# Kernel tuning notes

Measured on AMD Instinct MI355X. Metric: run time of the kernel, lower is better.

## Reference

```python
import jax, jax.numpy as jnp
import numpy as np


def setup_inputs() -> dict:
    key = jax.random.key(0)
    ks = jax.random.split(key, 16)
    B, C, H, W = 2, 64, 512, 512
    Nl, Nr = 100000, 20000

    def lin(k, fan_in, fan_out):
        kw, kb = jax.random.split(k)
        bound = 1.0 / np.sqrt(fan_in)
        w = jax.random.uniform(kw, (fan_in, fan_out), jnp.float32, -bound, bound)
        b = jax.random.uniform(kb, (fan_out,), jnp.float32, -bound, bound)
        return w, b

    w_lin, b_lin = lin(ks[0], 128, 64)
    w1, b1 = lin(ks[1], 128, 64)
    w2, b2 = lin(ks[2], 64, 32)
    w3, b3 = lin(ks[3], 32, 16)
    w4, b4 = lin(ks[4], 16, 1)

    return {
        "pc0_map": jax.random.normal(ks[5], (B, C, H, W), jnp.float32),
        "pc1_map": jax.random.normal(ks[6], (B, C, H, W), jnp.float32),
        "flow_map": jax.random.normal(ks[7], (B, C, H, W), jnp.float32),
        "lidar_coords": jax.random.randint(ks[8], (B, Nl, 3), 0, 512).astype(jnp.int64),
        "radar_coords": jax.random.randint(ks[9], (B, Nr, 3), 0, 512).astype(jnp.int64),
        "w_lin": w_lin, "b_lin": b_lin,
        "w1": w1, "b1": b1, "w2": w2, "b2": b2,
        "w3": w3, "b3": b3, "w4": w4, "b4": b4,
    }


def reference(pc0_map, pc1_map, flow_map, lidar_coords, radar_coords,
              w_lin, b_lin, w1, b1, w2, b2, w3, b3, w4, b4):
    gelu = lambda x: jax.nn.gelu(x, approximate=False)  # torch nn.GELU default (erf)

    def seg_single(p0, p1, fl, lc, rc):
        # lc: [Nl,3], rc: [Nr,3]; cat(lidar, radar) for all three maps
        coords = jnp.concatenate([lc, rc], axis=0)        # [N,3]
        r, c = coords[:, 1], coords[:, 2]
        f0 = p0[:, r, c].T                                # [N,64]
        f1 = p1[:, r, c].T                                # [N,64]
        ff = fl[:, r, c].T                                # [N,64]
        pc = jnp.concatenate([f0, f1], axis=1) @ w_lin + b_lin   # [N,64]
        h = jnp.concatenate([pc, ff], axis=1)             # [N,128]
        h = gelu(h @ w1 + b1)
        h = gelu(h @ w2 + b2)
        h = gelu(h @ w3 + b3)
        s = jax.nn.sigmoid(h @ w4 + b4)                   # [N,1]
        return s[:, 0]

    # [B, Nl+Nr] stacked (original returns a per-batch list; fixed N lets us stack)
    return jax.vmap(seg_single)(pc0_map, pc1_map, flow_map, lidar_coords, radar_coords)
```

## Files before the change

kernel.cpp:

```cpp
#include <hip/hip_runtime.h>
#include <math.h>

#define NPTS 120000
#define NLID 100000
#define NRAD 20000
#define NTOT (2 * NPTS)
#define MAPW 512
#define MAPHW (512 * 512)
#define NTILES 8192

typedef short sh8 __attribute__((ext_vector_type(8)));
typedef float f32x4 __attribute__((ext_vector_type(4)));
typedef unsigned short u16;
typedef unsigned int u32;

#define CSTR 70
#define H1S 72
#define H2S 40
#define H3S 24
#define HWAVE (16 * (H1S + H2S + H3S))

__device__ __forceinline__ float gelu_f(float x) {
    return 0.5f * x * (1.0f + erff(x * 0.7071067811865476f));
}
__device__ __forceinline__ u16 f2bf(float f) {
    unsigned int u = __float_as_uint(f);
    return (u16)((u + 0x7FFFu + ((u >> 16) & 1u)) >> 16);
}
__device__ __forceinline__ float bf2f(u16 h) {
    return __uint_as_float((unsigned int)h << 16);
}

__global__ void wprep_kernel(const float* __restrict__ w_lin, const float* __restrict__ b_lin,
                             const float* __restrict__ w1, const float* __restrict__ b1,
                             const float* __restrict__ w2, const float* __restrict__ w3,
                             u16* __restrict__ wfrag1, u16* __restrict__ wfrag2,
                             u16* __restrict__ wfrag3, float* __restrict__ b_eff) {
    int e = blockIdx.x * blockDim.x + threadIdx.x;
    if (e < 12288) {
        int fi = e >> 9, r = e & 511, lane = r >> 3, j = r & 7;
        int kk = fi >> 2, nt = fi & 3;
        int k = kk * 32 + (lane >> 4) * 8 + j;
        int n = nt * 16 + (lane & 15);
        float val;
        if (k < 128) {
            float s = 0.f;
            for (int jj = 0; jj < 64; jj++) s += w_lin[k * 64 + jj] * w1[jj * 64 + n];
            val = s;
        } else {
            val = w1[(k - 64) * 64 + n];
        }
        wfrag1[e] = f2bf(val);
    } else if (e < 12288 + 2048) {
        int e2 = e - 12288;
        int fi = e2 >> 9, lane = (e2 >> 3) & 63, j = e2 & 7;
        int kk = fi >> 1, nt = fi & 1;
        int k = kk * 32 + (lane >> 4) * 8 + j;
        int n = nt * 16 + (lane & 15);
        wfrag2[e2] = f2bf(w2[k * 32 + n]);
    } else if (e < 12288 + 2048 + 512) {
        int e3 = e - 12288 - 2048;
        int lane = e3 >> 3, j = e3 & 7;
        int k = (lane >> 4) * 8 + j;
        int n = lane & 15;
        wfrag3[e3] = f2bf(w3[k * 16 + n]);
    } else if (e < 12288 + 2048 + 512 + 64) {
        int n = e - 12288 - 2048 - 512;
        float s = b1[n];
        for (int jj = 0; jj < 64; jj++) s += b_lin[jj] * w1[jj * 64 + n];
        b_eff[n] = s;
    }
}

__global__ __launch_bounds__(256, 6) void fbseg_dense_kernel(
    const float* __restrict__ p0, const float* __restrict__ p1,
    const float* __restrict__ fl,
    const u16* __restrict__ wfrag1, const u16* __restrict__ wfrag2,
    const u16* __restrict__ wfrag3, const float* __restrict__ b_eff,
    const float* __restrict__ b2, const float* __restrict__ b3,
    const float* __restrict__ w4, const float* __restrict__ b4,
    float* __restrict__ score)
{
    __shared__ __align__(16) u16 feat[192 * CSTR];

    const int tid  = threadIdx.x;
    const int wv   = tid >> 6;
    const int lane = tid & 63;
    const int lr   = lane & 15;
    const int lq   = lane >> 4;
    const int m0w  = wv * 16;
    const int col  = m0w + lr;

    const int nb = blockIdx.x;
    const int b  = nb >> 12;
    const int r  = (nb & 4095) >> 3;
    const int c0 = (nb & 7) << 6;

    {
        const int q  = lq;
        const int p4 = lr * 4;
        const size_t goff = (size_t)b * ((size_t)64 * MAPHW)
                          + (size_t)r * MAPW + (size_t)(c0 + p4);
        #pragma unroll
        for (int s = 0; s < 12; s++) {
            const int C4 = wv * 48 + s * 4;
            const int C  = C4 + q;
            const float* mp = (C4 < 64) ? p0 : ((C4 < 128) ? p1 : fl);
            const f32x4 v = *(const f32x4*)(mp + goff + (size_t)(C & 63) * MAPHW);
            const u32 lo = ((u32)f2bf(v[1]) << 16) | (u32)f2bf(v[0]);
            const u32 hi = ((u32)f2bf(v[3]) << 16) | (u32)f2bf(v[2]);
            u32* dst = (u32*)(feat + C * CSTR + p4);
            dst[0] = lo;
            dst[1] = hi;
        }
    }
    __syncthreads();

    f32x4 acc1[4] = {};
    #pragma unroll
    for (int kk = 0; kk < 6; kk++) {
        sh8 a;
        u16* ap = (u16*)&a;
        #pragma unroll
        for (int j = 0; j < 8; j++)
            ap[j] = feat[(kk * 32 + lq * 8 + j) * CSTR + col];
        #pragma unroll
        for (int nt = 0; nt < 4; nt++) {
            sh8 bfr = *(const sh8*)(wfrag1 + ((kk * 4 + nt) * 64 + lane) * 8);
            acc1[nt] = __builtin_amdgcn_mfma_f32_16x16x32_bf16(a, bfr, acc1[nt], 0, 0, 0);
        }
    }
    __syncthreads();

    u16* Hbase = feat + wv * HWAVE;
    u16* H1w = Hbase;
    u16* H2w = Hbase + 16 * H1S;
    u16* H3w = Hbase + 16 * H1S + 16 * H2S;

    #pragma unroll
    for (int nt = 0; nt < 4; nt++) {
        const int n = nt * 16 + lr;
        const float bias = b_eff[n];
        #pragma unroll
        for (int rg = 0; rg < 4; rg++) {
            const int row = lq * 4 + rg;
            H1w[row * H1S + n] = f2bf(gelu_f(acc1[nt][rg] + bias));
        }
    }

    f32x4 acc2[2] = {};
    #pragma unroll
    for (int kk = 0; kk < 2; kk++) {
        sh8 a = *(const sh8*)&H1w[lr * H1S + kk * 32 + lq * 8];
        #pragma unroll
        for (int nt = 0; nt < 2; nt++) {
            sh8 bfr = *(const sh8*)(wfrag2 + ((kk * 2 + nt) * 64 + lane) * 8);
            acc2[nt] = __builtin_amdgcn_mfma_f32_16x16x32_bf16(a, bfr, acc2[nt], 0, 0, 0);
        }
    }
    #pragma unroll
    for (int nt = 0; nt < 2; nt++) {
        const int n = nt * 16 + lr;
        const float bias = b2[n];
        #pragma unroll
        for (int rg = 0; rg < 4; rg++) {
            const int row = lq * 4 + rg;
            H2w[row * H2S + n] = f2bf(gelu_f(acc2[nt][rg] + bias));
        }
    }

    f32x4 acc3 = {};
    {
        sh8 a = *(const sh8*)&H2w[lr * H2S + lq * 8];
        sh8 bfr = *(const sh8*)(wfrag3 + lane * 8);
        acc3 = __builtin_amdgcn_mfma_f32_16x16x32_bf16(a, bfr, acc3, 0, 0, 0);
    }
    {
        const float bias = b3[lr];
        #pragma unroll
        for (int rg = 0; rg < 4; rg++) {
            const int row = lq * 4 + rg;
            H3w[row * H3S + lr] = f2bf(gelu_f(acc3[rg] + bias));
        }
    }

    if (lane < 16) {
        float s = b4[0];
        #pragma unroll
        for (int k = 0; k < 16; k++) s = fmaf(bf2f(H3w[lane * H3S + k]), w4[k], s);
        score[(size_t)b * MAPHW + (size_t)r * MAPW + (size_t)(c0 + m0w + lane)] =
            1.0f / (1.0f + expf(-s));
    }
}

__global__ void lookup_kernel(const int* __restrict__ lidar, const int* __restrict__ radar,
                              const float* __restrict__ score, float* __restrict__ out) {
    int p = blockIdx.x * blockDim.x + threadIdx.x;
    if (p >= NTOT) return;
    int b = p / NPTS;
    int i = p - b * NPTS;
    int r, c;
    if (i < NLID) {
        const int* cd = lidar + (size_t)(b * NLID + i) * 3;
        r = cd[1]; c = cd[2];
    } else {
        const int* cd = radar + (size_t)(b * NRAD + (i - NLID)) * 3;
        r = cd[1]; c = cd[2];
    }
    out[p] = score[(size_t)b * MAPHW + (size_t)r * MAPW + (size_t)c];
}

extern "C" void kernel_launch(void* const* d_in, const int* in_sizes, int n_in,
                              void* d_out, int out_size, void* d_ws, size_t ws_size,
                              hipStream_t stream) {
    const float* p0    = (const float*)d_in[0];
    const float* p1    = (const float*)d_in[1];
    const float* fl    = (const float*)d_in[2];
    const int*   lidar = (const int*)d_in[3];
    const int*   radar = (const int*)d_in[4];
    const float* w_lin = (const float*)d_in[5];
    const float* b_lin = (const float*)d_in[6];
    const float* w1    = (const float*)d_in[7];
    const float* b1    = (const float*)d_in[8];
    const float* w2    = (const float*)d_in[9];
    const float* b2    = (const float*)d_in[10];
    const float* w3    = (const float*)d_in[11];
    const float* b3    = (const float*)d_in[12];
    const float* w4    = (const float*)d_in[13];
    const float* b4    = (const float*)d_in[14];
    float* out = (float*)d_out;

    char* ws = (char*)d_ws;
    float* score = (float*)ws;
    char* wbase  = ws + (size_t)2 * MAPHW * sizeof(float);
    u16*  wfrag1 = (u16*)wbase;
    u16*  wfrag2 = (u16*)(wbase + 12288 * 2);
    u16*  wfrag3 = (u16*)(wbase + (12288 + 2048) * 2);
    float* b_eff = (float*)(wbase + (12288 + 2048 + 512) * 2);

    hipLaunchKernelGGL(wprep_kernel, dim3((14912 + 255) / 256), dim3(256), 0, stream,
                       w_lin, b_lin, w1, b1, w2, w3, wfrag1, wfrag2, wfrag3, b_eff);
    hipLaunchKernelGGL(fbseg_dense_kernel, dim3(NTILES), dim3(256), 0, stream,
                       p0, p1, fl, wfrag1, wfrag2, wfrag3, b_eff, b2, b3, w4, b4, score);
    hipLaunchKernelGGL(lookup_kernel, dim3((NTOT + 255) / 256), dim3(256), 0, stream,
                       lidar, radar, score, out);
}
```

Before: 397.2 us.

## Load map tiles directly into LDS per wave and drop block barriers

Each wave now owns a 16-pixel tile and its own LDS slice. The map data is loaded with global_load_lds, so it goes straight to shared memory as fp32 instead of passing through registers and being converted to bf16 first, and the bf16 conversion moves to the MFMA operand gather. Removing the block-wide __syncthreads and the occupancy hint in launch_bounds lets waves run independently. The costs are a larger LDS footprint per block (48KB of fp32), which may limit occupancy, and a scalar fp32-to-bf16 conversion on every A-fragment element.

```diff
diff --git a/kernel.cpp b/kernel.cpp
--- a/kernel.cpp
+++ b/kernel.cpp
@@ -7,18 +7,18 @@
 #define NTOT (2 * NPTS)
 #define MAPW 512
 #define MAPHW (512 * 512)
-#define NTILES 8192
+#define NT16 32768
+#define NBLK (NT16 / 4)
 
 typedef short sh8 __attribute__((ext_vector_type(8)));
 typedef float f32x4 __attribute__((ext_vector_type(4)));
 typedef unsigned short u16;
 typedef unsigned int u32;
 
-#define CSTR 70
+#define WSLICE 3072
 #define H1S 72
 #define H2S 40
 #define H3S 24
-#define HWAVE (16 * (H1S + H2S + H3S))
 
 __device__ __forceinline__ float gelu_f(float x) {
     return 0.5f * x * (1.0f + erff(x * 0.7071067811865476f));
@@ -72,7 +72,7 @@
     }
 }
 
-__global__ __launch_bounds__(256, 6) void fbseg_dense_kernel(
+__global__ __launch_bounds__(256) void fbseg_dense_kernel(
     const float* __restrict__ p0, const float* __restrict__ p1,
     const float* __restrict__ fl,
     const u16* __restrict__ wfrag1, const u16* __restrict__ wfrag2,
@@ -81,40 +81,39 @@
     const float* __restrict__ w4, const float* __restrict__ b4,
     float* __restrict__ score)
 {
-    __shared__ __align__(16) u16 feat[192 * CSTR];
+    __shared__ __align__(16) float smem[4 * WSLICE];
 
     const int tid  = threadIdx.x;
     const int wv   = tid >> 6;
     const int lane = tid & 63;
     const int lr   = lane & 15;
     const int lq   = lane >> 4;
-    const int m0w  = wv * 16;
-    const int col  = m0w + lr;
-
-    const int nb = blockIdx.x;
-    const int b  = nb >> 12;
-    const int r  = (nb & 4095) >> 3;
-    const int c0 = (nb & 7) << 6;
+
+    const int idx = blockIdx.x * 4 + wv;
+    const int b   = idx >> 14;
+    const int r   = (idx >> 5) & 511;
+    const int c0  = (idx & 31) << 4;
+
+    float* feat = smem + wv * WSLICE;
 
     {
-        const int q  = lq;
-        const int p4 = lr * 4;
-        const size_t goff = (size_t)b * ((size_t)64 * MAPHW)
-                          + (size_t)r * MAPW + (size_t)(c0 + p4);
+        const int row_in = lane >> 2;
+        const int px4    = (lane & 3) << 2;
+        const size_t base = (size_t)b * ((size_t)64 * MAPHW)
+                          + (size_t)r * MAPW + (size_t)(c0 + px4);
         #pragma unroll
         for (int s = 0; s < 12; s++) {
-            const int C4 = wv * 48 + s * 4;
-            const int C  = C4 + q;
-            const float* mp = (C4 < 64) ? p0 : ((C4 < 128) ? p1 : fl);
-            const f32x4 v = *(const f32x4*)(mp + goff + (size_t)(C & 63) * MAPHW);
-            const u32 lo = ((u32)f2bf(v[1]) << 16) | (u32)f2bf(v[0]);
-            const u32 hi = ((u32)f2bf(v[3]) << 16) | (u32)f2bf(v[2]);
-            u32* dst = (u32*)(feat + C * CSTR + p4);
-            dst[0] = lo;
-            dst[1] = hi;
-        }
-    }
-    __syncthreads();
+            const float* mp = (s < 4) ? p0 : ((s < 8) ? p1 : fl);
+            const float* gp = mp + base + (size_t)(((s * 16) & 63) + row_in) * MAPHW;
+            const int dst = __builtin_amdgcn_readfirstlane(wv * WSLICE + s * 256);
+            __builtin_amdgcn_global_load_lds(
+                (const __attribute__((address_space(1))) u32*)gp,
+                (__attribute__((address_space(3))) u32*)(&smem[dst]),
+                16, 0, 0);
+        }
+        asm volatile("s_waitcnt vmcnt(0)" ::: "memory");
+        __builtin_amdgcn_sched_barrier(0);
+    }
 
     f32x4 acc1[4] = {};
     #pragma unroll
@@ -123,16 +122,15 @@
         u16* ap = (u16*)&a;
         #pragma unroll
         for (int j = 0; j < 8; j++)
-            ap[j] = feat[(kk * 32 + lq * 8 + j) * CSTR + col];
+            ap[j] = f2bf(feat[(kk * 32 + lq * 8 + j) * 16 + lr]);
         #pragma unroll
         for (int nt = 0; nt < 4; nt++) {
             sh8 bfr = *(const sh8*)(wfrag1 + ((kk * 4 + nt) * 64 + lane) * 8);
             acc1[nt] = __builtin_amdgcn_mfma_f32_16x16x32_bf16(a, bfr, acc1[nt], 0, 0, 0);
         }
     }
-    __syncthreads();
-
-    u16* Hbase = feat + wv * HWAVE;
+
+    u16* Hbase = (u16*)feat;
     u16* H1w = Hbase;
     u16* H2w = Hbase + 16 * H1S;
     u16* H3w = Hbase + 16 * H1S + 16 * H2S;
@@ -188,7 +186,7 @@
         float s = b4[0];
         #pragma unroll
         for (int k = 0; k < 16; k++) s = fmaf(bf2f(H3w[lane * H3S + k]), w4[k], s);
-        score[(size_t)b * MAPHW + (size_t)r * MAPW + (size_t)(c0 + m0w + lane)] =
+        score[(size_t)b * MAPHW + (size_t)r * MAPW + (size_t)(c0 + lane)] =
             1.0f / (1.0f + expf(-s));
     }
 }
@@ -240,7 +238,7 @@
 
     hipLaunchKernelGGL(wprep_kernel, dim3((14912 + 255) / 256), dim3(256), 0, stream,
                        w_lin, b_lin, w1, b1, w2, w3, wfrag1, wfrag2, wfrag3, b_eff);
-    hipLaunchKernelGGL(fbseg_dense_kernel, dim3(NTILES), dim3(256), 0, stream,
+    hipLaunchKernelGGL(fbseg_dense_kernel, dim3(NBLK), dim3(256), 0, stream,
                        p0, p1, fl, wfrag1, wfrag2, wfrag3, b_eff, b2, b3, w4, b4, score);
     hipLaunchKernelGGL(lookup_kernel, dim3((NTOT + 255) / 256), dim3(256), 0, stream,
                        lidar, radar, score, out);
```

New measurement: 408.7 us. 2.9% more time.
